# Kernel tuning notes

Measured on AMD Instinct MI355X. Metric: run time of the kernel, lower is better.

## Reference

```python
import jax, jax.numpy as jnp
import numpy as np

B, N, D, E, MULT = 4, 512, 1024, 8, 4
H = D * MULT
CAPACITY_FACTOR = 1.0
EPSILON = 1e-6


def setup_inputs() -> dict:
    key = jax.random.key(0)
    ks = jax.random.split(key, 4)
    s1 = 1.0 / np.sqrt(D)
    s2 = 1.0 / np.sqrt(H)
    return {
        "x": jax.random.normal(ks[0], (B, N, D), jnp.float32),
        "w_gate": jax.random.uniform(ks[1], (D, E), jnp.float32, -s1, s1),
        "b_gate": jnp.zeros((E,), jnp.float32),
        "w1": jax.random.uniform(ks[2], (E, D, H), jnp.float32, -s1, s1),
        "b1": jnp.zeros((E, H), jnp.float32),
        "w2": jax.random.uniform(ks[3], (E, H, D), jnp.float32, -s2, s2),
        "b2": jnp.zeros((E, D), jnp.float32),
    }


def _cv_squared(v):
    # torch: x.float().var() is unbiased (ddof=1)
    eps = 1e-10
    m = jnp.mean(v)
    return jnp.var(v, ddof=1) / (m * m + eps)


def reference(x, w_gate, b_gate, w1, b1, w2, b2):
    b, n, d = x.shape
    e = w_gate.shape[1]
    capacity = float(int(CAPACITY_FACTOR * b))  # int(capacity_factor * x.size(0))

    # SwitchGate
    gate = jax.nn.softmax(x @ w_gate + b_gate, axis=-1)          # [B,N,E]
    top_idx = jnp.argmax(gate, axis=-1)                          # [B,N]  == topk(1) indices
    # faithful to torch scatter_(dim=1, top_k_indices, 1): mask[bi, idx[bi,ni,0], 0] = 1
    mask = jnp.zeros_like(gate).at[jnp.arange(b)[:, None], top_idx, 0].set(1.0)
    masked = gate * mask
    denom = masked.sum(0, keepdims=True) + EPSILON               # [1,N,E]
    gate_scores = masked / denom * capacity                      # [B,N,E]
    importance = gate_scores.sum(0)                              # [N,E]
    load = (gate_scores > 0).sum(0).astype(jnp.float32)          # [N,E]
    loss = _cv_squared(importance) + _cv_squared(load)

    # Experts: FeedForward(dim, dim, mult) = Linear -> GELU(exact) -> Linear, all E at once
    h = jax.nn.gelu(jnp.einsum('bnd,edh->bneh', x, w1) + b1, approximate=False)  # [B,N,E,H]
    expert_out = jnp.einsum('bneh,ehd->bned', h, w2) + b2                        # [B,N,E,D]

    # moe_output = sum(gate_scores.unsqueeze(-2) * stacked_expert_outputs, dim=-1)
    out = jnp.einsum('bne,bned->bnd', gate_scores, expert_out)                   # [B,N,D]
    return out, loss
```

## Files before the change

### kernel.cpp

```cpp
#include <hip/hip_runtime.h>
#include <math.h>

static constexpr int Bb = 4;
static constexpr int Nn = 512;
static constexpr int Dd = 1024;
static constexpr int Ee = 8;
static constexpr int Hh = 4096;
static constexpr float CAP = 4.0f;
static constexpr float EPS = 1e-6f;

__global__ __launch_bounds__(256) void k_gate(
    const float* __restrict__ x, const float* __restrict__ wg,
    const float* __restrict__ bg, int* __restrict__ top,
    float* __restrict__ gate0, float* __restrict__ xT)
{
    __shared__ float swg[Ee * Dd];
    const int tid = threadIdx.x;
    for (int i = tid; i < Dd * Ee; i += 256) {
        int d = i >> 3, e = i & 7;
        swg[e * Dd + d] = wg[i];
    }
    __syncthreads();
    const int lane = tid & 63;
    const int tok = blockIdx.x * 4 + (tid >> 6);
    const float* xr = x + (size_t)tok * Dd;
    float acc[Ee];
#pragma unroll
    for (int e = 0; e < Ee; ++e) acc[e] = 0.f;
    for (int d = lane; d < Dd; d += 64) {
        float xv = xr[d];
#pragma unroll
        for (int e = 0; e < Ee; ++e) acc[e] += xv * swg[e * Dd + d];
    }
#pragma unroll
    for (int e = 0; e < Ee; ++e) {
        float v = acc[e];
#pragma unroll
        for (int off = 32; off > 0; off >>= 1) v += __shfl_xor(v, off, 64);
        acc[e] = v + bg[e];
    }
    const int n = tok & (Nn - 1);
    const int b = tok >> 9;
    if (n < 8) {
        const int t32 = b * 8 + n;
        for (int d = lane; d < Dd; d += 64) xT[d * 32 + t32] = xr[d];
    }
    if (lane == 0) {
        int best = 0;
        float bv = acc[0];
#pragma unroll
        for (int e = 1; e < Ee; ++e)
            if (acc[e] > bv) { bv = acc[e]; best = e; }
        top[tok] = best;
        if (n < 8) {
            float m = acc[0];
#pragma unroll
            for (int e = 1; e < Ee; ++e) m = fmaxf(m, acc[e]);
            float s = 0.f;
#pragma unroll
            for (int e = 0; e < Ee; ++e) s += expf(acc[e] - m);
            gate0[b * 8 + n] = expf(acc[0] - m) / s;
        }
    }
}

__global__ __launch_bounds__(64) void k_score(
    const int* __restrict__ top, const float* __restrict__ gate0,
    float* __restrict__ gs, float* __restrict__ loss_out)
{
    __shared__ int smask[Bb];
    const int tid = threadIdx.x;
    if (tid < Bb) smask[tid] = 0;
    __syncthreads();
    for (int i = tid; i < Bb * Nn; i += 64) {
        atomicOr(&smask[i >> 9], 1 << top[i]);
    }
    __syncthreads();
    if (tid == 0) {
        float imp[8], ld[8], gsl[32];
        for (int n = 0; n < 8; ++n) {
            float mv[4];
            float den = 0.f;
            for (int b = 0; b < 4; ++b) {
                float g = ((smask[b] >> n) & 1) ? gate0[b * 8 + n] : 0.f;
                mv[b] = g;
                den += g;
            }
            den += EPS;
            float s = 0.f, cnt = 0.f;
            for (int b = 0; b < 4; ++b) {
                float v = mv[b] / den * CAP;
                gsl[b * 8 + n] = v;
                s += v;
                if (v > 0.f) cnt += 1.f;
            }
            imp[n] = s;
            ld[n] = cnt;
        }
        for (int i = 0; i < 32; ++i) gs[i] = gsl[i];
        const float M = (float)(Nn * Ee);
        float si = 0.f, sl = 0.f;
        for (int n = 0; n < 8; ++n) { si += imp[n]; sl += ld[n]; }
        const float mi = si / M, ml = sl / M;
        float di = 0.f, dl = 0.f;
        for (int n = 0; n < 8; ++n) {
            di += (imp[n] - mi) * (imp[n] - mi);
            dl += (ld[n] - ml) * (ld[n] - ml);
        }
        di += (M - 8.f) * mi * mi;
        dl += (M - 8.f) * ml * ml;
        const float vi = di / (M - 1.f), vl = dl / (M - 1.f);
        *loss_out = vi / (mi * mi + 1e-10f) + vl / (ml * ml + 1e-10f);
    }
}

__global__ __launch_bounds__(256) void k_ffn1(
    const float* __restrict__ w1, const float* __restrict__ xT,
    float* __restrict__ p1)
{
    const int tid = threadIdx.x;
    const int h = blockIdx.x * 256 + tid;
    const int k0 = blockIdx.y * 64;
    const float* w = w1 + (size_t)k0 * Hh + h;
    const float* xk = xT + k0 * 32;
    float acc[32];
#pragma unroll
    for (int t = 0; t < 32; ++t) acc[t] = 0.f;
    for (int k = 0; k < 64; ++k) {
        float wv = *w;
        w += Hh;
#pragma unroll
        for (int t = 0; t < 32; ++t) acc[t] = fmaf(xk[t], wv, acc[t]);
        xk += 32;
    }
    float* o = p1 + ((size_t)blockIdx.y * 32) * Hh + h;
#pragma unroll
    for (int t = 0; t < 32; ++t) { *o = acc[t]; o += Hh; }
}

__global__ __launch_bounds__(256) void k_h(
    const float* __restrict__ p1, const float* __restrict__ b1,
    float* __restrict__ hT)
{
    const int idx = blockIdx.x * 256 + threadIdx.x;
    const int hh = idx & (Hh - 1);
    const int t = idx >> 12;
    float s = b1[hh];
#pragma unroll
    for (int q = 0; q < 16; ++q)
        s += p1[((size_t)(q * 32 + t)) * Hh + hh];
    hT[(size_t)hh * 32 + t] = 0.5f * s * (1.f + erff(s * 0.70710678118654752440f));
}

__global__ __launch_bounds__(256) void k_ffn2(
    const float* __restrict__ w2, const float* __restrict__ hT,
    float* __restrict__ p2)
{
    const int tid = threadIdx.x;
    const int d = blockIdx.x * 256 + tid;
    const int k0 = blockIdx.y * 64;
    const float* w = w2 + (size_t)k0 * Dd + d;
    const float* hk = hT + k0 * 32;
    float acc[32];
#pragma unroll
    for (int t = 0; t < 32; ++t) acc[t] = 0.f;
    for (int k = 0; k < 64; ++k) {
        float wv = *w;
        w += Dd;
#pragma unroll
        for (int t = 0; t < 32; ++t) acc[t] = fmaf(hk[t], wv, acc[t]);
        hk += 32;
    }
    float* o = p2 + ((size_t)blockIdx.y * 32) * Dd + d;
#pragma unroll
    for (int t = 0; t < 32; ++t) { *o = acc[t]; o += Dd; }
}

__global__ __launch_bounds__(256) void k_out(
    const float* __restrict__ p2, const float* __restrict__ b2,
    const float* __restrict__ gs, float* __restrict__ out)
{
    const int row = blockIdx.x;
    const int d4 = threadIdx.x * 4;
    const int n = row & (Nn - 1);
    float4 o = make_float4(0.f, 0.f, 0.f, 0.f);
    if (n < 8) {
        const int b = row >> 9;
        const int t = b * 8 + n;
        const float g = gs[t];
        float4 a = make_float4(0.f, 0.f, 0.f, 0.f);
        const float* p = p2 + (size_t)t * Dd + d4;
#pragma unroll 8
        for (int s = 0; s < 64; ++s) {
            float4 v = *(const float4*)p;
            p += (size_t)32 * Dd;
            a.x += v.x; a.y += v.y; a.z += v.z; a.w += v.w;
        }
        float4 bb = *(const float4*)(b2 + d4);
        o.x = g * (a.x + bb.x);
        o.y = g * (a.y + bb.y);
        o.z = g * (a.z + bb.z);
        o.w = g * (a.w + bb.w);
    }
    *(float4*)(out + (size_t)row * Dd + d4) = o;
}

extern "C" void kernel_launch(void* const* d_in, const int* in_sizes, int n_in,
                              void* d_out, int out_size, void* d_ws, size_t ws_size,
                              hipStream_t stream) {
    const float* x  = (const float*)d_in[0];
    const float* wg = (const float*)d_in[1];
    const float* bg = (const float*)d_in[2];
    const float* w1 = (const float*)d_in[3];
    const float* b1 = (const float*)d_in[4];
    const float* w2 = (const float*)d_in[5];
    const float* b2 = (const float*)d_in[6];
    float* out = (float*)d_out;

    float* wsf   = (float*)d_ws;
    int*   top   = (int*)d_ws;
    float* gate0 = wsf + 2048;
    float* gs    = wsf + 2080;
    float* xT    = wsf + 4096;
    float* hT    = wsf + 36864;
    float* p1    = wsf + 167936;
    float* p2    = wsf + 2265088;

    k_gate<<<dim3(Bb * Nn / 4), dim3(256), 0, stream>>>(x, wg, bg, top, gate0, xT);
    k_score<<<dim3(1), dim3(64), 0, stream>>>(top, gate0, gs, out + (out_size - 1));
    k_ffn1<<<dim3(16, 16), dim3(256), 0, stream>>>(w1, xT, p1);
    k_h<<<dim3(512), dim3(256), 0, stream>>>(p1, b1, hT);
    k_ffn2<<<dim3(4, 64), dim3(256), 0, stream>>>(w2, hT, p2);
    k_out<<<dim3(Bb * Nn), dim3(256), 0, stream>>>(p2, b2, gs, out);
}
```

Before: 300.9 us.

## Stage activations in LDS, batch weight loads, fuse mask reduction into gate

The FFN kernels now stage the small transposed activation tile in shared memory and batch-prefetch 16 weight rows into registers before the FMA loop. ffn1 gains float2 weight loads and a finer K split (32 slices), which doubles the partial-sum buffer read by k_h. The gate kernel vectorizes its dot product with a padded LDS layout and ORs the top-expert mask directly with global atomics, so k_score no longer scans all tokens, at the cost of an added memset. The larger p1 split adds workspace traffic and more reduction work in k_h.

```diff
diff --git a/kernel.cpp b/kernel.cpp
--- a/kernel.cpp
+++ b/kernel.cpp
@@ -9,16 +9,19 @@
 static constexpr float CAP = 4.0f;
 static constexpr float EPS = 1e-6f;
 
+static constexpr int P1S = 32;
+static constexpr int P2S = 64;
+
 __global__ __launch_bounds__(256) void k_gate(
     const float* __restrict__ x, const float* __restrict__ wg,
-    const float* __restrict__ bg, int* __restrict__ top,
+    const float* __restrict__ bg, int* __restrict__ smask,
     float* __restrict__ gate0, float* __restrict__ xT)
 {
-    __shared__ float swg[Ee * Dd];
+    __shared__ float swg[Ee * 1028];
     const int tid = threadIdx.x;
     for (int i = tid; i < Dd * Ee; i += 256) {
         int d = i >> 3, e = i & 7;
-        swg[e * Dd + d] = wg[i];
+        swg[e * 1028 + d] = wg[i];
     }
     __syncthreads();
     const int lane = tid & 63;
@@ -27,10 +30,18 @@
     float acc[Ee];
 #pragma unroll
     for (int e = 0; e < Ee; ++e) acc[e] = 0.f;
-    for (int d = lane; d < Dd; d += 64) {
-        float xv = xr[d];
-#pragma unroll
-        for (int e = 0; e < Ee; ++e) acc[e] += xv * swg[e * Dd + d];
+#pragma unroll
+    for (int j = 0; j < 4; ++j) {
+        const int d0 = j * 256 + lane * 4;
+        float4 xv = *(const float4*)(xr + d0);
+#pragma unroll
+        for (int e = 0; e < Ee; ++e) {
+            float4 wv = *(const float4*)(&swg[e * 1028 + d0]);
+            acc[e] = fmaf(xv.x, wv.x, acc[e]);
+            acc[e] = fmaf(xv.y, wv.y, acc[e]);
+            acc[e] = fmaf(xv.z, wv.z, acc[e]);
+            acc[e] = fmaf(xv.w, wv.w, acc[e]);
+        }
     }
 #pragma unroll
     for (int e = 0; e < Ee; ++e) {
@@ -51,7 +62,7 @@
 #pragma unroll
         for (int e = 1; e < Ee; ++e)
             if (acc[e] > bv) { bv = acc[e]; best = e; }
-        top[tok] = best;
+        atomicOr(&smask[b], 1 << best);
         if (n < 8) {
             float m = acc[0];
 #pragma unroll
@@ -65,18 +76,10 @@
 }
 
 __global__ __launch_bounds__(64) void k_score(
-    const int* __restrict__ top, const float* __restrict__ gate0,
+    const int* __restrict__ smask, const float* __restrict__ gate0,
     float* __restrict__ gs, float* __restrict__ loss_out)
 {
-    __shared__ int smask[Bb];
-    const int tid = threadIdx.x;
-    if (tid < Bb) smask[tid] = 0;
-    __syncthreads();
-    for (int i = tid; i < Bb * Nn; i += 64) {
-        atomicOr(&smask[i >> 9], 1 << top[i]);
-    }
-    __syncthreads();
-    if (tid == 0) {
+    if (threadIdx.x == 0) {
         float imp[8], ld[8], gsl[32];
         for (int n = 0; n < 8; ++n) {
             float mv[4];
@@ -118,24 +121,46 @@
     const float* __restrict__ w1, const float* __restrict__ xT,
     float* __restrict__ p1)
 {
+    __shared__ float xs[32 * 32];
     const int tid = threadIdx.x;
-    const int h = blockIdx.x * 256 + tid;
-    const int k0 = blockIdx.y * 64;
-    const float* w = w1 + (size_t)k0 * Hh + h;
-    const float* xk = xT + k0 * 32;
-    float acc[32];
-#pragma unroll
-    for (int t = 0; t < 32; ++t) acc[t] = 0.f;
-    for (int k = 0; k < 64; ++k) {
-        float wv = *w;
-        w += Hh;
-#pragma unroll
-        for (int t = 0; t < 32; ++t) acc[t] = fmaf(xk[t], wv, acc[t]);
-        xk += 32;
+    {
+        float4 v = *(const float4*)(xT + blockIdx.y * (32 * 32) + tid * 4);
+        *(float4*)(xs + tid * 4) = v;
+    }
+    __syncthreads();
+    const int h = blockIdx.x * 512 + tid * 2;
+    const int k0 = blockIdx.y * 32;
+    const float* wp = w1 + (size_t)k0 * Hh + h;
+    float2 acc[32];
+#pragma unroll
+    for (int t = 0; t < 32; ++t) acc[t] = make_float2(0.f, 0.f);
+#pragma unroll
+    for (int half = 0; half < 2; ++half) {
+        float2 wbuf[16];
+#pragma unroll
+        for (int kk = 0; kk < 16; ++kk)
+            wbuf[kk] = *(const float2*)(wp + (size_t)(half * 16 + kk) * Hh);
+#pragma unroll
+        for (int kk = 0; kk < 16; ++kk) {
+            const float4* xrow = (const float4*)(xs + (half * 16 + kk) * 32);
+            const float2 w = wbuf[kk];
+#pragma unroll
+            for (int t4 = 0; t4 < 8; ++t4) {
+                float4 xv = xrow[t4];
+                acc[t4 * 4 + 0].x = fmaf(xv.x, w.x, acc[t4 * 4 + 0].x);
+                acc[t4 * 4 + 0].y = fmaf(xv.x, w.y, acc[t4 * 4 + 0].y);
+                acc[t4 * 4 + 1].x = fmaf(xv.y, w.x, acc[t4 * 4 + 1].x);
+                acc[t4 * 4 + 1].y = fmaf(xv.y, w.y, acc[t4 * 4 + 1].y);
+                acc[t4 * 4 + 2].x = fmaf(xv.z, w.x, acc[t4 * 4 + 2].x);
+                acc[t4 * 4 + 2].y = fmaf(xv.z, w.y, acc[t4 * 4 + 2].y);
+                acc[t4 * 4 + 3].x = fmaf(xv.w, w.x, acc[t4 * 4 + 3].x);
+                acc[t4 * 4 + 3].y = fmaf(xv.w, w.y, acc[t4 * 4 + 3].y);
+            }
+        }
     }
     float* o = p1 + ((size_t)blockIdx.y * 32) * Hh + h;
 #pragma unroll
-    for (int t = 0; t < 32; ++t) { *o = acc[t]; o += Hh; }
+    for (int t = 0; t < 32; ++t) { *(float2*)o = acc[t]; o += Hh; }
 }
 
 __global__ __launch_bounds__(256) void k_h(
@@ -147,7 +172,7 @@
     const int t = idx >> 12;
     float s = b1[hh];
 #pragma unroll
-    for (int q = 0; q < 16; ++q)
+    for (int q = 0; q < P1S; ++q)
         s += p1[((size_t)(q * 32 + t)) * Hh + hh];
     hT[(size_t)hh * 32 + t] = 0.5f * s * (1.f + erff(s * 0.70710678118654752440f));
 }
@@ -156,20 +181,40 @@
     const float* __restrict__ w2, const float* __restrict__ hT,
     float* __restrict__ p2)
 {
+    __shared__ float hs[64 * 32];
     const int tid = threadIdx.x;
+    {
+        float4 v0 = *(const float4*)(hT + blockIdx.y * (64 * 32) + tid * 8);
+        float4 v1 = *(const float4*)(hT + blockIdx.y * (64 * 32) + tid * 8 + 4);
+        *(float4*)(hs + tid * 8) = v0;
+        *(float4*)(hs + tid * 8 + 4) = v1;
+    }
+    __syncthreads();
     const int d = blockIdx.x * 256 + tid;
     const int k0 = blockIdx.y * 64;
-    const float* w = w2 + (size_t)k0 * Dd + d;
-    const float* hk = hT + k0 * 32;
+    const float* wp = w2 + (size_t)k0 * Dd + d;
     float acc[32];
 #pragma unroll
     for (int t = 0; t < 32; ++t) acc[t] = 0.f;
-    for (int k = 0; k < 64; ++k) {
-        float wv = *w;
-        w += Dd;
-#pragma unroll
-        for (int t = 0; t < 32; ++t) acc[t] = fmaf(hk[t], wv, acc[t]);
-        hk += 32;
+#pragma unroll
+    for (int q = 0; q < 4; ++q) {
+        float wbuf[16];
+#pragma unroll
+        for (int kk = 0; kk < 16; ++kk)
+            wbuf[kk] = wp[(size_t)(q * 16 + kk) * Dd];
+#pragma unroll
+        for (int kk = 0; kk < 16; ++kk) {
+            const float4* xrow = (const float4*)(hs + (q * 16 + kk) * 32);
+            const float w = wbuf[kk];
+#pragma unroll
+            for (int t4 = 0; t4 < 8; ++t4) {
+                float4 xv = xrow[t4];
+                acc[t4 * 4 + 0] = fmaf(xv.x, w, acc[t4 * 4 + 0]);
+                acc[t4 * 4 + 1] = fmaf(xv.y, w, acc[t4 * 4 + 1]);
+                acc[t4 * 4 + 2] = fmaf(xv.z, w, acc[t4 * 4 + 2]);
+                acc[t4 * 4 + 3] = fmaf(xv.w, w, acc[t4 * 4 + 3]);
+            }
+        }
     }
     float* o = p2 + ((size_t)blockIdx.y * 32) * Dd + d;
 #pragma unroll
@@ -191,7 +236,7 @@
         float4 a = make_float4(0.f, 0.f, 0.f, 0.f);
         const float* p = p2 + (size_t)t * Dd + d4;
 #pragma unroll 8
-        for (int s = 0; s < 64; ++s) {
+        for (int s = 0; s < P2S; ++s) {
             float4 v = *(const float4*)p;
             p += (size_t)32 * Dd;
             a.x += v.x; a.y += v.y; a.z += v.z; a.w += v.w;
@@ -218,18 +263,19 @@
     float* out = (float*)d_out;
 
     float* wsf   = (float*)d_ws;
-    int*   top   = (int*)d_ws;
-    float* gate0 = wsf + 2048;
-    float* gs    = wsf + 2080;
-    float* xT    = wsf + 4096;
+    int*   smask = (int*)d_ws;
+    float* gate0 = wsf + 64;
+    float* gs    = wsf + 128;
+    float* xT    = wsf + 256;
     float* hT    = wsf + 36864;
     float* p1    = wsf + 167936;
-    float* p2    = wsf + 2265088;
-
-    k_gate<<<dim3(Bb * Nn / 4), dim3(256), 0, stream>>>(x, wg, bg, top, gate0, xT);
-    k_score<<<dim3(1), dim3(64), 0, stream>>>(top, gate0, gs, out + (out_size - 1));
-    k_ffn1<<<dim3(16, 16), dim3(256), 0, stream>>>(w1, xT, p1);
+    float* p2    = wsf + 4362240;
+
+    hipMemsetAsync(smask, 0, 4 * sizeof(int), stream);
+    k_gate<<<dim3(Bb * Nn / 4), dim3(256), 0, stream>>>(x, wg, bg, smask, gate0, xT);
+    k_score<<<dim3(1), dim3(64), 0, stream>>>(smask, gate0, gs, out + (out_size - 1));
+    k_ffn1<<<dim3(8, P1S), dim3(256), 0, stream>>>(w1, xT, p1);
     k_h<<<dim3(512), dim3(256), 0, stream>>>(p1, b1, hT);
-    k_ffn2<<<dim3(4, 64), dim3(256), 0, stream>>>(w2, hT, p2);
+    k_ffn2<<<dim3(4, P2S), dim3(256), 0, stream>>>(w2, hT, p2);
     k_out<<<dim3(Bb * Nn), dim3(256), 0, stream>>>(p2, b2, gs, out);
 }
```

Result: no change. 300.3 us (-0.2%).
